# Optimization experiments

Hardware: AMD Instinct MI355X
Metric: run time of the kernel (lower is better)

Reference implementation:

```python
import jax, jax.numpy as jnp
import numpy as np

N = 8192      # num nodes
D = 256       # input feature dim (num_embeddings)
F_OUT = 128   # out_channels
B = 4096      # lookup batch size


def setup_inputs() -> dict:
    key = jax.random.key(0)
    k1, k2, k3, k4 = jax.random.split(key, 4)
    x = jax.random.randint(k1, (B,), 0, N)                      # node ids for final lookup
    adj = jax.random.randint(k2, (N, N), 0, 2).astype(jnp.int32)  # dense 0/1 adjacency
    embedding = jax.random.normal(k3, (N, D), dtype=jnp.float32)
    xavier = 1.414 * (6.0 / (D + F_OUT)) ** 0.5
    W = jax.random.uniform(k4, (D, F_OUT), minval=-xavier, maxval=xavier, dtype=jnp.float32)
    return {"x": x, "adj": adj, "embedding": embedding, "W": W}


def reference(x, adj, embedding, W):
    Wh = embedding @ W                                   # [N, F_OUT]
    mask = adj > 0
    maskf = mask.astype(Wh.dtype)
    # per-row neighbor mean of Wh (vectorized form of the python row loop)
    deg = jnp.maximum(jnp.sum(maskf, axis=1), 1.0)       # guard; random adj has deg>0
    neigh_mean = (maskf @ Wh) / deg[:, None]             # [N, F_OUT]
    alpha = jnp.sum(Wh * neigh_mean, axis=1)             # [N], Wh[i] . mean(neighbors)
    e = Wh @ Wh.T + alpha[:, None]                       # similarity + row-wise query term
    att = jax.nn.softmax(jnp.where(mask, e, jnp.asarray(-9e15, e.dtype)), axis=1)
    # dropout is identity in eval mode (p effectively 0)
    h_prime = att @ Wh                                   # [N, F_OUT]
    emb_out = jax.nn.elu(h_prime)                        # concat=True branch
    out = emb_out[x]                                     # F.embedding lookup, [B, F_OUT]
    nrm = jnp.linalg.norm(out, axis=1, keepdims=True)
    return out / jnp.maximum(nrm, 1e-12)                 # F.normalize (L2, eps=1e-12)
```

## Files before the change

kernel.cpp:

```cpp
#include <hip/hip_runtime.h>

#define NN 8192
#define DD 256
#define FF 128
#define BB 4096
#define NSPLIT 8
#define KCHUNK (NN / NSPLIT)
#define QBLKS 128

typedef unsigned short ushortT;
typedef __attribute__((ext_vector_type(8))) short bf16x8;
typedef __attribute__((ext_vector_type(4))) float f32x4;

__device__ __forceinline__ ushortT f2bf(float f) {
  unsigned u = __float_as_uint(f);
  return (ushortT)((u + 0x7FFFu + ((u >> 16) & 1u)) >> 16);
}
__device__ __forceinline__ float bf2f(ushortT h) {
  return __uint_as_float(((unsigned)h) << 16);
}


__global__ __launch_bounds__(256) void init_kernel(int* flags, int* cnt) {
  int i = blockIdx.x * 256 + threadIdx.x;
  flags[i] = 0;
  if (i == 0) *cnt = 0;
}

__global__ __launch_bounds__(256) void scatter_kernel(const int* __restrict__ x, int* flags) {
  int b = blockIdx.x * 256 + threadIdx.x;
  flags[x[b]] = 1;
}

__global__ __launch_bounds__(256) void compact_kernel(const int* __restrict__ flags, int* cnt,
                                                      int* list, int* slot) {
  int i = blockIdx.x * 256 + threadIdx.x;
  if (flags[i]) {
    int pos = atomicAdd(cnt, 1);
    list[pos] = i;
    slot[i] = pos;
  }
}


__global__ __launch_bounds__(256) void wh_kernel(const float* __restrict__ emb,
                                                 const float* __restrict__ W,
                                                 ushortT* __restrict__ Whh,
                                                 ushortT* __restrict__ Whl) {
  __shared__ float Es[32 * 65];
  __shared__ float Ws[64 * 128];
  const int t = threadIdx.x;
  const int r0 = blockIdx.x * 32;
  const int rg = t >> 5;
  const int cg = t & 31;
  float4 acc[4] = {{0,0,0,0},{0,0,0,0},{0,0,0,0},{0,0,0,0}};
  for (int kc = 0; kc < DD; kc += 64) {
    __syncthreads();
    for (int i = 0; i < 8; ++i) {
      int idx = t + 256 * i;
      int r = idx >> 6, k = idx & 63;
      Es[r * 65 + k] = emb[(r0 + r) * DD + kc + k];
    }
    for (int i = 0; i < 8; ++i) {
      int idx = t + 256 * i;
      int kr = idx >> 5, c4 = (idx & 31) * 4;
      *(float4*)&Ws[kr * 128 + c4] = *(const float4*)&W[(kc + kr) * 128 + c4];
    }
    __syncthreads();
    for (int k = 0; k < 64; ++k) {
      float4 b = *(const float4*)&Ws[k * 128 + cg * 4];
#pragma unroll
      for (int i = 0; i < 4; ++i) {
        float a = Es[(rg * 4 + i) * 65 + k];
        acc[i].x += a * b.x; acc[i].y += a * b.y;
        acc[i].z += a * b.z; acc[i].w += a * b.w;
      }
    }
  }
#pragma unroll
  for (int i = 0; i < 4; ++i) {
    int row = r0 + rg * 4 + i;
    float v[4] = {acc[i].x, acc[i].y, acc[i].z, acc[i].w};
    ushort4 hh, ll;
    ushortT* hp = (ushortT*)&hh;
    ushortT* lp = (ushortT*)&ll;
#pragma unroll
    for (int k = 0; k < 4; ++k) {
      ushortT h = f2bf(v[k]);
      hp[k] = h;
      lp[k] = f2bf(v[k] - bf2f(h));
    }
    *(ushort4*)&Whh[row * FF + cg * 4] = hh;
    *(ushort4*)&Whl[row * FF + cg * 4] = ll;
  }
}


__global__ __launch_bounds__(256) void transpose_kernel(const ushortT* __restrict__ A,
                                                        ushortT* __restrict__ At) {
  __shared__ ushortT tile[128 * 136];
  const int t = threadIdx.x;
  const int r0 = blockIdx.x * 128;
  for (int i = 0; i < 8; ++i) {
    int idx = t + 256 * i;
    int r = idx >> 4, c8 = idx & 15;
    *(bf16x8*)&tile[r * 136 + c8 * 8] = *(const bf16x8*)&A[(r0 + r) * FF + c8 * 8];
  }
  __syncthreads();
  for (int i = 0; i < 8; ++i) {
    int idx = t + 256 * i;
    int f = idx >> 4, r8 = idx & 15;
    bf16x8 v;
#pragma unroll
    for (int u = 0; u < 8; ++u) v[u] = (short)tile[(r8 * 8 + u) * 136 + f];
    *(bf16x8*)&At[(size_t)f * NN + r0 + r8 * 8] = v;
  }
}


__global__ __launch_bounds__(256) void attn_kernel(
    const ushortT* __restrict__ Whh, const ushortT* __restrict__ Whl,
    const ushortT* __restrict__ WhT, const int* __restrict__ adj,
    const int* __restrict__ list, const int* __restrict__ cntp,
    float* __restrict__ Opart, float* __restrict__ mpart, float* __restrict__ lpart) {
  __shared__ short Ps[8 * 32 * 8];
  __shared__ float pm[2][32];
  __shared__ float lsum[32];
  __shared__ float mrow[32], lrow[32];
  __shared__ int nid[32];

  const int t = threadIdx.x;
  const int cnt = *cntp;
  const int qblk = blockIdx.x >> 3, chunk = blockIdx.x & 7;
  const int qbase = qblk * 32;
  if (qbase >= cnt) return;

  if (t < 32) {
    nid[t] = list[min(qbase + t, cnt - 1)];
    mrow[t] = -1e30f;
    lrow[t] = 0.f;
  }
  __syncthreads();

  const int w = t >> 6, l = t & 63, quad = l >> 4, c = l & 15;
  const int mt = w >> 1, nth = w & 1;
  const int koff = quad * 8;

  const size_t qrow = (size_t)nid[mt * 16 + c] * FF;
  bf16x8 qh[4], ql[4];
#pragma unroll
  for (int ks = 0; ks < 4; ++ks) {
    qh[ks] = *(const bf16x8*)(Whh + qrow + ks * 32 + koff);
    ql[ks] = *(const bf16x8*)(Whl + qrow + ks * 32 + koff);
  }
  size_t arow[4];
#pragma unroll
  for (int r = 0; r < 4; ++r) arow[r] = (size_t)nid[mt * 16 + quad * 4 + r] * NN;

  f32x4 O[4] = {{0,0,0,0},{0,0,0,0},{0,0,0,0},{0,0,0,0}};
  const int kt0 = chunk * KCHUNK;

  for (int kt = kt0; kt < kt0 + KCHUNK; kt += 64) {
    __syncthreads();
    int av[2][4];
#pragma unroll
    for (int nt2 = 0; nt2 < 2; ++nt2) {
      int ck = kt + (nth * 2 + nt2) * 16 + c;
#pragma unroll
      for (int r = 0; r < 4; ++r) av[nt2][r] = adj[arow[r] + ck];
    }
    f32x4 sacc[2];
#pragma unroll
    for (int nt2 = 0; nt2 < 2; ++nt2) {
      int nt = nth * 2 + nt2;
      const ushortT* kh = Whh + (size_t)(kt + nt * 16 + c) * FF + koff;
      const ushortT* kl = Whl + (size_t)(kt + nt * 16 + c) * FF + koff;
      f32x4 a = {0, 0, 0, 0};
#pragma unroll
      for (int ks = 0; ks < 4; ++ks) {
        bf16x8 bh = *(const bf16x8*)(kh + ks * 32);
        bf16x8 bl = *(const bf16x8*)(kl + ks * 32);
        a = __builtin_amdgcn_mfma_f32_16x16x32_bf16(qh[ks], bh, a, 0, 0, 0);
        a = __builtin_amdgcn_mfma_f32_16x16x32_bf16(ql[ks], bh, a, 0, 0, 0);
        a = __builtin_amdgcn_mfma_f32_16x16x32_bf16(qh[ks], bl, a, 0, 0, 0);
      }
      sacc[nt2] = a;
    }
    float rmax[4];
#pragma unroll
    for (int r = 0; r < 4; ++r) {
      float v0 = av[0][r] > 0 ? sacc[0][r] : -1e30f;
      float v1 = av[1][r] > 0 ? sacc[1][r] : -1e30f;
      rmax[r] = fmaxf(v0, v1);
    }
#pragma unroll
    for (int mk = 1; mk <= 8; mk <<= 1)
#pragma unroll
      for (int r = 0; r < 4; ++r) rmax[r] = fmaxf(rmax[r], __shfl_xor(rmax[r], mk, 16));
    if (c == 0) {
#pragma unroll
      for (int r = 0; r < 4; ++r) pm[nth][mt * 16 + quad * 4 + r] = rmax[r];
    }
    if (t < 32) lsum[t] = 0.f;
    __syncthreads();
    if (t < 32) {
      float nm = fmaxf(mrow[t], fmaxf(pm[0][t], pm[1][t]));
      pm[0][t] = __expf(mrow[t] - nm);
      mrow[t] = nm;
    }
    __syncthreads();
    float psl[4];
#pragma unroll
    for (int r = 0; r < 4; ++r) {
      int q = mt * 16 + quad * 4 + r;
      float nm = mrow[q];
      float pr[2];
#pragma unroll
      for (int nt2 = 0; nt2 < 2; ++nt2) {
        float p = av[nt2][r] > 0 ? __expf(sacc[nt2][r] - nm) : 0.f;
        ushortT pb = f2bf(p);
        int key = (nth * 2 + nt2) * 16 + c;
        int cb = key >> 3;
        int g = cb * 32 + (q ^ (cb & 7));
        Ps[g * 8 + (key & 7)] = (short)pb;
        pr[nt2] = bf2f(pb);
      }
      psl[r] = pr[0] + pr[1];
    }
    float scr[4];
#pragma unroll
    for (int r = 0; r < 4; ++r) scr[r] = pm[0][mt * 16 + quad * 4 + r];
#pragma unroll
    for (int i = 0; i < 4; ++i)
#pragma unroll
      for (int r = 0; r < 4; ++r) O[i][r] *= scr[r];
#pragma unroll
    for (int mk = 1; mk <= 8; mk <<= 1)
#pragma unroll
      for (int r = 0; r < 4; ++r) psl[r] += __shfl_xor(psl[r], mk, 16);
    if (c == 0) {
#pragma unroll
      for (int r = 0; r < 4; ++r) atomicAdd(&lsum[mt * 16 + quad * 4 + r], psl[r]);
    }
    __syncthreads();
    if (t < 32) lrow[t] = lrow[t] * pm[0][t] + lsum[t];
    bf16x8 pa[2];
#pragma unroll
    for (int ks2 = 0; ks2 < 2; ++ks2) {
      int cb = ks2 * 4 + quad;
      int g = cb * 32 + ((mt * 16 + c) ^ (cb & 7));
      pa[ks2] = *(const bf16x8*)&Ps[g * 8];
    }
#pragma unroll
    for (int i = 0; i < 4; ++i) {
      int ft = nth * 4 + i;
      const ushortT* vp = WhT + (size_t)(ft * 16 + c) * NN + kt;
#pragma unroll
      for (int ks2 = 0; ks2 < 2; ++ks2) {
        bf16x8 vb = *(const bf16x8*)(vp + ks2 * 32 + koff);
        O[i] = __builtin_amdgcn_mfma_f32_16x16x32_bf16(pa[ks2], vb, O[i], 0, 0, 0);
      }
    }
  }
  float* Op = Opart + (size_t)chunk * 4096 * FF;
#pragma unroll
  for (int i = 0; i < 4; ++i) {
    int ft = nth * 4 + i;
#pragma unroll
    for (int r = 0; r < 4; ++r)
      Op[(size_t)(qbase + mt * 16 + quad * 4 + r) * FF + ft * 16 + c] = O[i][r];
  }
  if (t < 32) {
    mpart[chunk * 4096 + qbase + t] = mrow[t];
    lpart[chunk * 4096 + qbase + t] = lrow[t];
  }
}


__global__ __launch_bounds__(128) void combine_kernel(
    const float* __restrict__ Opart, const float* __restrict__ mpart,
    const float* __restrict__ lpart, float* __restrict__ h) {
  const int r = blockIdx.x;
  const int t = threadIdx.x;
  float mstar = -1e30f;
#pragma unroll
  for (int c = 0; c < NSPLIT; ++c) mstar = fmaxf(mstar, mpart[c * 4096 + r]);
  float lstar = 0.f, acc = 0.f;
#pragma unroll
  for (int c = 0; c < NSPLIT; ++c) {
    float wgt = __expf(mpart[c * 4096 + r] - mstar);
    lstar += wgt * lpart[c * 4096 + r];
    acc += wgt * Opart[((size_t)c * 4096 + r) * FF + t];
  }
  float v = acc / fmaxf(lstar, 1e-30f);
  h[r * FF + t] = v > 0.f ? v : expm1f(v);
}


__global__ __launch_bounds__(128) void out_kernel(const int* __restrict__ x,
                                                  const int* __restrict__ slot,
                                                  const float* __restrict__ h,
                                                  float* __restrict__ out) {
  const int b = blockIdx.x, t = threadIdx.x;
  const int s = slot[x[b]];
  float v = h[s * FF + t];
  float ss = v * v;
#pragma unroll
  for (int wd = 1; wd <= 32; wd <<= 1) ss += __shfl_xor(ss, wd);
  __shared__ float red[2];
  if ((t & 63) == 0) red[t >> 6] = ss;
  __syncthreads();
  float tot = red[0] + red[1];
  float scale = 1.f / fmaxf(sqrtf(tot), 1e-12f);
  out[b * FF + t] = v * scale;
}


extern "C" void kernel_launch(void* const* d_in, const int* in_sizes, int n_in,
                              void* d_out, int out_size, void* d_ws, size_t ws_size,
                              hipStream_t stream) {
  const int*   x   = (const int*)d_in[0];
  const int*   adj = (const int*)d_in[1];
  const float* emb = (const float*)d_in[2];
  const float* W   = (const float*)d_in[3];
  float* out = (float*)d_out;

  char* base = (char*)d_ws;
  ushortT* Whh = (ushortT*)(base);
  ushortT* Whl = (ushortT*)(base + 2097152);
  float*   h   = (float*)(base + 2097152);
  ushortT* WhT = (ushortT*)(base + 4194304);
  float* Opart = (float*)(base + 6291456);
  float* mpart = (float*)(base + 23068672);
  float* lpart = (float*)(base + 23199744);
  int*   flags = (int*)(base + 23330816);
  int*   list  = (int*)(base + 23363584);
  int*   slot  = (int*)(base + 23379968);
  int*   cnt   = (int*)(base + 23412736);
  (void)in_sizes; (void)n_in; (void)out_size; (void)ws_size;

  hipLaunchKernelGGL(init_kernel,      dim3(NN / 256), dim3(256), 0, stream, flags, cnt);
  hipLaunchKernelGGL(scatter_kernel,   dim3(BB / 256), dim3(256), 0, stream, x, flags);
  hipLaunchKernelGGL(compact_kernel,   dim3(NN / 256), dim3(256), 0, stream, flags, cnt, list, slot);
  hipLaunchKernelGGL(wh_kernel,        dim3(NN / 32),  dim3(256), 0, stream, emb, W, Whh, Whl);
  hipLaunchKernelGGL(transpose_kernel, dim3(NN / 128), dim3(256), 0, stream, Whh, WhT);
  hipLaunchKernelGGL(attn_kernel,      dim3(QBLKS * NSPLIT), dim3(256), 0, stream,
                     Whh, Whl, WhT, adj, list, cnt, Opart, mpart, lpart);
  hipLaunchKernelGGL(combine_kernel,   dim3(4096), dim3(128), 0, stream, Opart, mpart, lpart, h);
  hipLaunchKernelGGL(out_kernel,       dim3(BB),   dim3(128), 0, stream, x, slot, h, out);
}
```

Before: 532.5 us.

## Restructure attention kernel to single-wave blocks with register-resident softmax state

Rewrites the flash-style attention kernel so each 64-thread block (one wave) handles 16 query rows over a key chunk, replacing the previous 4-wave 32-row blocks. Running max and sum now live in registers and are reduced with lane shuffles, which removes the several __syncthreads, LDS atomics and shared-memory softmax bookkeeping done every 64-key step. Each wave now computes all 4 key tiles and all 8 output feature tiles itself. The trade-off is a higher per-thread register load (8 output accumulators, 4 score tiles) and a doubled grid. Each block also no longer shares Wh key and value reads across waves, which may raise cache traffic.

```diff
diff --git a/kernel.cpp b/kernel.cpp
--- a/kernel.cpp
+++ b/kernel.cpp
@@ -6,7 +6,6 @@
 #define BB 4096
 #define NSPLIT 8
 #define KCHUNK (NN / NSPLIT)
-#define QBLKS 128
 
 typedef unsigned short ushortT;
 typedef __attribute__((ext_vector_type(8))) short bf16x8;
@@ -118,63 +117,54 @@
 }
 
 
-__global__ __launch_bounds__(256) void attn_kernel(
+__global__ __launch_bounds__(64) void attn_kernel(
     const ushortT* __restrict__ Whh, const ushortT* __restrict__ Whl,
     const ushortT* __restrict__ WhT, const int* __restrict__ adj,
     const int* __restrict__ list, const int* __restrict__ cntp,
     float* __restrict__ Opart, float* __restrict__ mpart, float* __restrict__ lpart) {
-  __shared__ short Ps[8 * 32 * 8];
-  __shared__ float pm[2][32];
-  __shared__ float lsum[32];
-  __shared__ float mrow[32], lrow[32];
-  __shared__ int nid[32];
-
-  const int t = threadIdx.x;
+  __shared__ short Ps[16 * 72];
   const int cnt = *cntp;
-  const int qblk = blockIdx.x >> 3, chunk = blockIdx.x & 7;
-  const int qbase = qblk * 32;
-  if (qbase >= cnt) return;
-
-  if (t < 32) {
-    nid[t] = list[min(qbase + t, cnt - 1)];
-    mrow[t] = -1e30f;
-    lrow[t] = 0.f;
-  }
-  __syncthreads();
-
-  const int w = t >> 6, l = t & 63, quad = l >> 4, c = l & 15;
-  const int mt = w >> 1, nth = w & 1;
-  const int koff = quad * 8;
-
-  const size_t qrow = (size_t)nid[mt * 16 + c] * FF;
+  const int qt = blockIdx.x >> 3;
+  const int chunk = blockIdx.x & 7;
+  const int q0 = qt * 16;
+  if (q0 >= cnt) return;
+
+  const int l = threadIdx.x;
+  const int quad = l >> 4, c = l & 15;
+
+  const int qidc = list[min(q0 + c, cnt - 1)];
+  const ushortT* qph = Whh + (size_t)qidc * FF + quad * 8;
+  const ushortT* qpl = Whl + (size_t)qidc * FF + quad * 8;
   bf16x8 qh[4], ql[4];
 #pragma unroll
   for (int ks = 0; ks < 4; ++ks) {
-    qh[ks] = *(const bf16x8*)(Whh + qrow + ks * 32 + koff);
-    ql[ks] = *(const bf16x8*)(Whl + qrow + ks * 32 + koff);
+    qh[ks] = *(const bf16x8*)(qph + ks * 32);
+    ql[ks] = *(const bf16x8*)(qpl + ks * 32);
   }
   size_t arow[4];
 #pragma unroll
-  for (int r = 0; r < 4; ++r) arow[r] = (size_t)nid[mt * 16 + quad * 4 + r] * NN;
-
-  f32x4 O[4] = {{0,0,0,0},{0,0,0,0},{0,0,0,0},{0,0,0,0}};
+  for (int r = 0; r < 4; ++r)
+    arow[r] = (size_t)list[min(q0 + quad * 4 + r, cnt - 1)] * NN;
+
+  float m[4], lr[4];
+#pragma unroll
+  for (int r = 0; r < 4; ++r) { m[r] = -1e30f; lr[r] = 0.f; }
+  f32x4 O[8] = {{0,0,0,0},{0,0,0,0},{0,0,0,0},{0,0,0,0},
+                {0,0,0,0},{0,0,0,0},{0,0,0,0},{0,0,0,0}};
+
   const int kt0 = chunk * KCHUNK;
-
   for (int kt = kt0; kt < kt0 + KCHUNK; kt += 64) {
-    __syncthreads();
-    int av[2][4];
-#pragma unroll
-    for (int nt2 = 0; nt2 < 2; ++nt2) {
-      int ck = kt + (nth * 2 + nt2) * 16 + c;
-#pragma unroll
-      for (int r = 0; r < 4; ++r) av[nt2][r] = adj[arow[r] + ck];
-    }
-    f32x4 sacc[2];
-#pragma unroll
-    for (int nt2 = 0; nt2 < 2; ++nt2) {
-      int nt = nth * 2 + nt2;
-      const ushortT* kh = Whh + (size_t)(kt + nt * 16 + c) * FF + koff;
-      const ushortT* kl = Whl + (size_t)(kt + nt * 16 + c) * FF + koff;
+    int av[4][4];
+#pragma unroll
+    for (int nt = 0; nt < 4; ++nt)
+#pragma unroll
+      for (int r = 0; r < 4; ++r) av[nt][r] = adj[arow[r] + kt + nt * 16 + c];
+
+    f32x4 sacc[4];
+#pragma unroll
+    for (int nt = 0; nt < 4; ++nt) {
+      const ushortT* kh = Whh + (size_t)(kt + nt * 16 + c) * FF + quad * 8;
+      const ushortT* kl = Whl + (size_t)(kt + nt * 16 + c) * FF + quad * 8;
       f32x4 a = {0, 0, 0, 0};
 #pragma unroll
       for (int ks = 0; ks < 4; ++ks) {
@@ -184,95 +174,76 @@
         a = __builtin_amdgcn_mfma_f32_16x16x32_bf16(ql[ks], bh, a, 0, 0, 0);
         a = __builtin_amdgcn_mfma_f32_16x16x32_bf16(qh[ks], bl, a, 0, 0, 0);
       }
-      sacc[nt2] = a;
-    }
+      sacc[nt] = a;
+    }
+
     float rmax[4];
 #pragma unroll
     for (int r = 0; r < 4; ++r) {
-      float v0 = av[0][r] > 0 ? sacc[0][r] : -1e30f;
-      float v1 = av[1][r] > 0 ? sacc[1][r] : -1e30f;
-      rmax[r] = fmaxf(v0, v1);
+      float v = -1e30f;
+#pragma unroll
+      for (int nt = 0; nt < 4; ++nt) v = fmaxf(v, av[nt][r] > 0 ? sacc[nt][r] : -1e30f);
+      rmax[r] = v;
     }
 #pragma unroll
     for (int mk = 1; mk <= 8; mk <<= 1)
 #pragma unroll
       for (int r = 0; r < 4; ++r) rmax[r] = fmaxf(rmax[r], __shfl_xor(rmax[r], mk, 16));
-    if (c == 0) {
-#pragma unroll
-      for (int r = 0; r < 4; ++r) pm[nth][mt * 16 + quad * 4 + r] = rmax[r];
-    }
-    if (t < 32) lsum[t] = 0.f;
-    __syncthreads();
-    if (t < 32) {
-      float nm = fmaxf(mrow[t], fmaxf(pm[0][t], pm[1][t]));
-      pm[0][t] = __expf(mrow[t] - nm);
-      mrow[t] = nm;
-    }
-    __syncthreads();
-    float psl[4];
+    float sc[4], psum[4];
 #pragma unroll
     for (int r = 0; r < 4; ++r) {
-      int q = mt * 16 + quad * 4 + r;
-      float nm = mrow[q];
-      float pr[2];
-#pragma unroll
-      for (int nt2 = 0; nt2 < 2; ++nt2) {
-        float p = av[nt2][r] > 0 ? __expf(sacc[nt2][r] - nm) : 0.f;
+      float nm = fmaxf(m[r], rmax[r]);
+      sc[r] = __expf(m[r] - nm);
+      m[r] = nm;
+      psum[r] = 0.f;
+    }
+#pragma unroll
+    for (int nt = 0; nt < 4; ++nt)
+#pragma unroll
+      for (int r = 0; r < 4; ++r) {
+        float p = av[nt][r] > 0 ? __expf(sacc[nt][r] - m[r]) : 0.f;
         ushortT pb = f2bf(p);
-        int key = (nth * 2 + nt2) * 16 + c;
-        int cb = key >> 3;
-        int g = cb * 32 + (q ^ (cb & 7));
-        Ps[g * 8 + (key & 7)] = (short)pb;
-        pr[nt2] = bf2f(pb);
+        Ps[(quad * 4 + r) * 72 + nt * 16 + c] = (short)pb;
+        psum[r] += bf2f(pb);
       }
-      psl[r] = pr[0] + pr[1];
-    }
-    float scr[4];
-#pragma unroll
-    for (int r = 0; r < 4; ++r) scr[r] = pm[0][mt * 16 + quad * 4 + r];
-#pragma unroll
-    for (int i = 0; i < 4; ++i)
-#pragma unroll
-      for (int r = 0; r < 4; ++r) O[i][r] *= scr[r];
 #pragma unroll
     for (int mk = 1; mk <= 8; mk <<= 1)
 #pragma unroll
-      for (int r = 0; r < 4; ++r) psl[r] += __shfl_xor(psl[r], mk, 16);
-    if (c == 0) {
-#pragma unroll
-      for (int r = 0; r < 4; ++r) atomicAdd(&lsum[mt * 16 + quad * 4 + r], psl[r]);
-    }
-    __syncthreads();
-    if (t < 32) lrow[t] = lrow[t] * pm[0][t] + lsum[t];
+      for (int r = 0; r < 4; ++r) psum[r] += __shfl_xor(psum[r], mk, 16);
+#pragma unroll
+    for (int r = 0; r < 4; ++r) lr[r] = lr[r] * sc[r] + psum[r];
+
+#pragma unroll
+    for (int ft = 0; ft < 8; ++ft)
+#pragma unroll
+      for (int r = 0; r < 4; ++r) O[ft][r] *= sc[r];
     bf16x8 pa[2];
 #pragma unroll
-    for (int ks2 = 0; ks2 < 2; ++ks2) {
-      int cb = ks2 * 4 + quad;
-      int g = cb * 32 + ((mt * 16 + c) ^ (cb & 7));
-      pa[ks2] = *(const bf16x8*)&Ps[g * 8];
-    }
-#pragma unroll
-    for (int i = 0; i < 4; ++i) {
-      int ft = nth * 4 + i;
-      const ushortT* vp = WhT + (size_t)(ft * 16 + c) * NN + kt;
+    for (int ks2 = 0; ks2 < 2; ++ks2)
+      pa[ks2] = *(const bf16x8*)&Ps[c * 72 + ks2 * 32 + quad * 8];
+#pragma unroll
+    for (int ft = 0; ft < 8; ++ft) {
+      const ushortT* vp = WhT + (size_t)(ft * 16 + c) * NN + kt + quad * 8;
 #pragma unroll
       for (int ks2 = 0; ks2 < 2; ++ks2) {
-        bf16x8 vb = *(const bf16x8*)(vp + ks2 * 32 + koff);
-        O[i] = __builtin_amdgcn_mfma_f32_16x16x32_bf16(pa[ks2], vb, O[i], 0, 0, 0);
+        bf16x8 vb = *(const bf16x8*)(vp + ks2 * 32);
+        O[ft] = __builtin_amdgcn_mfma_f32_16x16x32_bf16(pa[ks2], vb, O[ft], 0, 0, 0);
       }
     }
   }
+
   float* Op = Opart + (size_t)chunk * 4096 * FF;
 #pragma unroll
-  for (int i = 0; i < 4; ++i) {
-    int ft = nth * 4 + i;
+  for (int ft = 0; ft < 8; ++ft)
 #pragma unroll
     for (int r = 0; r < 4; ++r)
-      Op[(size_t)(qbase + mt * 16 + quad * 4 + r) * FF + ft * 16 + c] = O[i][r];
-  }
-  if (t < 32) {
-    mpart[chunk * 4096 + qbase + t] = mrow[t];
-    lpart[chunk * 4096 + qbase + t] = lrow[t];
+      Op[(size_t)(q0 + quad * 4 + r) * FF + ft * 16 + c] = O[ft][r];
+  if (c == 0) {
+#pragma unroll
+    for (int r = 0; r < 4; ++r) {
+      mpart[chunk * 4096 + q0 + quad * 4 + r] = m[r];
+      lpart[chunk * 4096 + q0 + quad * 4 + r] = lr[r];
+    }
   }
 }
 
@@ -344,7 +315,7 @@
   hipLaunchKernelGGL(compact_kernel,   dim3(NN / 256), dim3(256), 0, stream, flags, cnt, list, slot);
   hipLaunchKernelGGL(wh_kernel,        dim3(NN / 32),  dim3(256), 0, stream, emb, W, Whh, Whl);
   hipLaunchKernelGGL(transpose_kernel, dim3(NN / 128), dim3(256), 0, stream, Whh, WhT);
-  hipLaunchKernelGGL(attn_kernel,      dim3(QBLKS * NSPLIT), dim3(256), 0, stream,
+  hipLaunchKernelGGL(attn_kernel,      dim3((BB / 16) * NSPLIT), dim3(64), 0, stream,
                      Whh, Whl, WhT, adj, list, cnt, Opart, mpart, lpart);
   hipLaunchKernelGGL(combine_kernel,   dim3(4096), dim3(128), 0, stream, Opart, mpart, lpart, h);
   hipLaunchKernelGGL(out_kernel,       dim3(BB),   dim3(128), 0, stream, x, slot, h, out);
```

Result: faster. 514.1 us (-3.4%).
